# Optimization experiments

Hardware: AMD Instinct MI355X
Metric: run time of the kernel (lower is better)

The kernel has to match this reference:

```python
import jax, jax.numpy as jnp
import numpy as np

NEG_SLOPE = 0.2
EPS = 1e-5

N_NODES = 50000
N_GRAPHS = 500
NODES_PER_GRAPH = 100
N_EDGES = 500000
F_IN = 16
F_GRAPH = 4
HID = 64
N_CLASSES = 2


def setup_inputs() -> dict:
    key = jax.random.key(0)
    ks = jax.random.split(key, 32)
    x = jax.random.normal(ks[0], (N_NODES, F_IN), dtype=jnp.float32)
    # intra-graph random edges: dst lives in the same 100-node block as src
    src = jax.random.randint(ks[1], (N_EDGES,), 0, N_NODES)
    dst = (src // NODES_PER_GRAPH) * NODES_PER_GRAPH + jax.random.randint(ks[2], (N_EDGES,), 0, NODES_PER_GRAPH)
    edge_index = jnp.stack([src, dst]).astype(jnp.int64)
    graph_input = jax.random.normal(ks[3], (N_GRAPHS, F_GRAPH), dtype=jnp.float32)
    batch = (jnp.arange(N_NODES) // NODES_PER_GRAPH).astype(jnp.int64)

    def w(k, shape, scale=0.1):
        return (jax.random.normal(k, shape, dtype=jnp.float32) * scale)

    inp = dict(x=x, edge_index=edge_index, graph_input=graph_input, batch=batch)
    # GraphNorm params
    inp['gn_w'] = jnp.ones((F_IN,), jnp.float32)
    inp['gn_b'] = w(ks[4], (F_IN,))
    inp['gn_ms'] = jnp.ones((F_IN,), jnp.float32)
    inp['W1'] = w(ks[5], (F_IN, 4 * HID))
    inp['as1'] = w(ks[6], (4, HID)); inp['ad1'] = w(ks[7], (4, HID))
    inp['b1'] = w(ks[8], (4 * HID,))
    inp['W2'] = w(ks[9], (4 * HID, 4 * HID))
    inp['as2'] = w(ks[10], (4, HID)); inp['ad2'] = w(ks[11], (4, HID))
    inp['b2'] = w(ks[12], (4 * HID,))
    inp['W3'] = w(ks[13], (4 * HID, HID))
    inp['as3'] = w(ks[14], (1, HID)); inp['ad3'] = w(ks[15], (1, HID))
    inp['b3'] = w(ks[16], (HID,))
    # BatchNorm1d (eval mode) over [HID + F_GRAPH]
    D = HID + F_GRAPH
    inp['bn_g'] = 1.0 + w(ks[17], (D,))
    inp['bn_b'] = w(ks[18], (D,))
    inp['bn_m'] = jnp.zeros((D,), jnp.float32)
    inp['bn_v'] = jnp.ones((D,), jnp.float32)
    # Dense head
    inp['Wd1'] = w(ks[19], (D, HID)); inp['bd1'] = w(ks[20], (HID,))
    inp['Wd2'] = w(ks[21], (HID, HID)); inp['bd2'] = w(ks[22], (HID,))
    inp['Wo'] = w(ks[23], (HID, N_CLASSES)); inp['bo'] = w(ks[24], (N_CLASSES,))
    return inp


def _segment_softmax(e, seg, n):
    m = jax.ops.segment_max(e, seg, num_segments=n)
    ex = jnp.exp(e - m[seg])
    s = jax.ops.segment_sum(ex, seg, num_segments=n)
    return ex / s[seg]


def _gat_conv(x, src, dst, W, att_src, att_dst, b):
    N = x.shape[0]
    H, C = att_src.shape
    loop = jnp.arange(N)
    src = jnp.concatenate([src, loop])  # PyG GATConv adds self-loops
    dst = jnp.concatenate([dst, loop])
    h = (x @ W).reshape(N, H, C)
    a_src = (h * att_src).sum(-1)  # [N,H]
    a_dst = (h * att_dst).sum(-1)
    e = jax.nn.leaky_relu(a_src[src] + a_dst[dst], NEG_SLOPE)  # [E,H]
    alpha = _segment_softmax(e, dst, N)
    out = jax.ops.segment_sum(h[src] * alpha[:, :, None], dst, num_segments=N)
    return out.reshape(N, H * C) + b


def _graph_norm(x, batch, n_graphs, w, b, ms):
    cnt = jax.ops.segment_sum(jnp.ones((x.shape[0],), x.dtype), batch, num_segments=n_graphs)[:, None]
    mean = jax.ops.segment_sum(x, batch, num_segments=n_graphs) / cnt
    out = x - mean[batch] * ms
    var = jax.ops.segment_sum(out * out, batch, num_segments=n_graphs) / cnt
    return w * out / jnp.sqrt(var[batch] + EPS) + b


def _global_mean_pool(x, batch, n_graphs):
    cnt = jax.ops.segment_sum(jnp.ones((x.shape[0],), x.dtype), batch, num_segments=n_graphs)[:, None]
    return jax.ops.segment_sum(x, batch, num_segments=n_graphs) / cnt


def reference(x, edge_index, graph_input, batch,
              gn_w, gn_b, gn_ms,
              W1, as1, ad1, b1,
              W2, as2, ad2, b2,
              W3, as3, ad3, b3,
              bn_g, bn_b, bn_m, bn_v,
              Wd1, bd1, Wd2, bd2, Wo, bo):
    src, dst = edge_index[0], edge_index[1]
    G = graph_input.shape[0]
    h = _graph_norm(x, batch, G, gn_w, gn_b, gn_ms)
    # dropout is a no-op in eval
    h = jax.nn.elu(_gat_conv(h, src, dst, W1, as1, ad1, b1))
    h = jax.nn.elu(_gat_conv(h, src, dst, W2, as2, ad2, b2))
    h = _gat_conv(h, src, dst, W3, as3, ad3, b3)
    g = _global_mean_pool(h, batch, G)
    g = jnp.concatenate([g, graph_input], axis=1)
    g = (g - bn_m) / jnp.sqrt(bn_v + EPS) * bn_g + bn_b  # BatchNorm1d eval
    g = jax.nn.selu(g @ Wd1 + bd1)
    g = jax.nn.selu(g @ Wd2 + bd2)
    g = g @ Wo + bo
    return jax.nn.softmax(g, axis=1)
```

## Files before the change

kernel.cpp:

```cpp
#include <hip/hip_runtime.h>
#include <math.h>

#define N_NODES 50000
#define N_ROWS_PAD 50048
#define N_GRAPHS 500
#define NPG 100
#define N_EDGES 500000
#define F_IN 16
#define HID 64
#define EW_CAP 1408

#define SELU_SCALE 1.0507009873554804934193349852946f
#define SELU_ALPHA 1.6732632423543772848170429916717f

typedef __attribute__((ext_vector_type(8))) short short8;
typedef __attribute__((ext_vector_type(8))) unsigned short ushort8;
typedef __attribute__((ext_vector_type(4))) float floatx4;

__device__ __forceinline__ float lrelu(float x){ return x > 0.f ? x : 0.2f * x; }
__device__ __forceinline__ float eluf(float x){ return x > 0.f ? x : expf(x) - 1.f; }
__device__ __forceinline__ float seluf(float x){
    return x > 0.f ? SELU_SCALE * x : SELU_SCALE * (SELU_ALPHA * (expf(x) - 1.f));
}
__device__ __forceinline__ unsigned short f2bf(float x){
    unsigned u = __float_as_uint(x);
    return (unsigned short)((u + 0x7FFFu + ((u >> 16) & 1u)) >> 16);
}
__device__ __forceinline__ float bf2f(unsigned short u){
    return __uint_as_float((unsigned)u << 16);
}
__device__ __forceinline__ float bf2f_lo(unsigned u){
    return __uint_as_float(u << 16);
}
__device__ __forceinline__ float bf2f_hi(unsigned u){
    return __uint_as_float(u & 0xFFFF0000u);
}

__global__ void k_count(const int* __restrict__ dst, int* __restrict__ counts){
    int e = blockIdx.x * 256 + threadIdx.x;
    if (e < N_EDGES) atomicAdd(&counts[dst[e]], 1);
}

__global__ void __launch_bounds__(128)
k_local_scan(const int* __restrict__ counts, int* __restrict__ noff,
             int* __restrict__ cnt, int* __restrict__ write_ptr){
    __shared__ int s[128];
    int g = blockIdx.x, t = threadIdx.x;
    int v = (t < NPG) ? counts[g * NPG + t] : 0;
    s[t] = v; __syncthreads();
    for (int o = 1; o < 128; o <<= 1){
        int x = (t >= o) ? s[t - o] : 0;
        __syncthreads();
        s[t] += x;
        __syncthreads();
    }
    if (t < NPG){
        int excl = s[t] - v;
        noff[g * NPG + t] = excl;
        cnt[g * NPG + t] = v;
        write_ptr[g * NPG + t] = excl;
    }
}

__global__ void k_scatter(const int* __restrict__ src, const int* __restrict__ dst,
                          int* __restrict__ write_ptr, unsigned* __restrict__ csr){
    int e = blockIdx.x * 256 + threadIdx.x;
    if (e < N_EDGES){
        int d = dst[e];
        int g = d / NPG;
        int b = g * NPG;
        int pos = atomicAdd(&write_ptr[d], 1);
        csr[(size_t)g * EW_CAP + pos] = (unsigned)((src[e] - b) | ((d - b) << 8));
    }
}

__global__ void k_prep(const float* __restrict__ W1, const float* __restrict__ as1,
                       const float* __restrict__ ad1,
                       const float* __restrict__ W2, const float* __restrict__ as2,
                       const float* __restrict__ ad2,
                       const float* __restrict__ W3, const float* __restrict__ as3,
                       const float* __restrict__ ad3,
                       unsigned short* __restrict__ Wp2, unsigned short* __restrict__ Wp3,
                       float* __restrict__ M1f,
                       unsigned short* __restrict__ Mp2, unsigned short* __restrict__ Mp3){
    int id = blockIdx.x * 256 + threadIdx.x;
    if (id < 65536){
        int k = id >> 8, o = id & 255;
        int srccol = (o & 3) * 64 + (o >> 2);
        Wp2[(((k >> 3) * 256) + o) * 8 + (k & 7)] = f2bf(W2[k * 256 + srccol]);
    } else if (id < 81920){
        int i = id - 65536;
        int k = i >> 6, n = i & 63;
        Wp3[(((k >> 3) * 64) + n) * 8 + (k & 7)] = f2bf(W3[i]);
    } else if (id < 82048){
        int i = id - 81920;
        int k = i >> 3, j = i & 7;
        int h = j & 3;
        const float* a = (j < 4) ? as1 : ad1;
        float s = 0.f;
        for (int c = 0; c < 64; c++) s += W1[k * 256 + h * 64 + c] * a[h * 64 + c];
        M1f[k * 8 + j] = s;
    } else if (id < 86144){
        int i = id - 82048;
        int k = i >> 4, col = i & 15;
        float s = 0.f;
        if (col < 8){
            int h = col & 3;
            const float* a = (col < 4) ? as2 : ad2;
            for (int c = 0; c < 64; c++) s += W2[k * 256 + h * 64 + c] * a[h * 64 + c];
        }
        Mp2[((k >> 3) * 16 + col) * 8 + (k & 7)] = f2bf(s);
    } else if (id < 90240){
        int i = id - 86144;
        int k = i >> 4, col = i & 15;
        float s = 0.f;
        if (col < 2){
            const float* a = (col == 0) ? as3 : ad3;
            for (int c = 0; c < 64; c++) s += W3[k * 64 + c] * a[c];
        }
        Mp3[((k >> 3) * 16 + col) * 8 + (k & 7)] = f2bf(s);
    }
}

__global__ void __launch_bounds__(256)
k_gnorm_conv1(const float* __restrict__ x, const float* __restrict__ w,
              const float* __restrict__ b, const float* __restrict__ ms,
              const float* __restrict__ W1, const float* __restrict__ M1f,
              unsigned short* __restrict__ Ybf, float* __restrict__ lg1){
    __shared__ float sx[NPG * F_IN];
    __shared__ float Ws[16][256];
    __shared__ float red[16][16];
    __shared__ float meanS[16], varS[16];
    int g = blockIdx.x, t = threadIdx.x;
    int base = g * NPG;
    for (int idx = t; idx < NPG * F_IN; idx += 256) sx[idx] = x[base * F_IN + idx];
    for (int i = t; i < 1024; i += 256)
        *(float4*)&Ws[0][i * 4] = *(const float4*)&W1[i * 4];
    __syncthreads();
    int f = t & 15, grp = t >> 4;
    float p = 0.f;
    for (int i = grp; i < NPG; i += 16) p += sx[i * 16 + f];
    red[grp][f] = p; __syncthreads();
    if (t < 16){
        float s = 0.f;
        for (int i = 0; i < 16; i++) s += red[i][t];
        meanS[t] = s * (1.f / 100.f);
    }
    __syncthreads();
    float mm = meanS[f] * ms[f];
    p = 0.f;
    for (int i = grp; i < NPG; i += 16){ float v = sx[i * 16 + f] - mm; p += v * v; }
    red[grp][f] = p; __syncthreads();
    if (t < 16){
        float s = 0.f;
        for (int i = 0; i < 16; i++) s += red[i][t];
        varS[t] = s * (1.f / 100.f);
    }
    __syncthreads();
    for (int idx = t; idx < NPG * F_IN; idx += 256){
        int ff = idx & 15;
        sx[idx] = w[ff] * (sx[idx] - meanS[ff] * ms[ff]) * rsqrtf(varS[ff] + 1e-5f) + b[ff];
    }
    __syncthreads();
    int c4 = t & 15, rsub = t >> 4;
    for (int n = rsub; n < NPG; n += 16){
        float acc[16];
        #pragma unroll
        for (int j = 0; j < 16; j++) acc[j] = 0.f;
        #pragma unroll
        for (int k = 0; k < 16; k++){
            float a_ = sx[n * 16 + k];
            float4 b0 = *(const float4*)&Ws[k][c4 * 4];
            float4 b1 = *(const float4*)&Ws[k][64 + c4 * 4];
            float4 b2 = *(const float4*)&Ws[k][128 + c4 * 4];
            float4 b3 = *(const float4*)&Ws[k][192 + c4 * 4];
            float bv[16] = {b0.x, b0.y, b0.z, b0.w, b1.x, b1.y, b1.z, b1.w,
                            b2.x, b2.y, b2.z, b2.w, b3.x, b3.y, b3.z, b3.w};
            #pragma unroll
            for (int j = 0; j < 16; j++) acc[j] = fmaf(a_, bv[j], acc[j]);
        }
        ushort8 ua, ub;
        #pragma unroll
        for (int m = 0; m < 8; m++){
            ua[m] = f2bf(acc[(m & 3) * 4 + (m >> 2)]);
            ub[m] = f2bf(acc[(m & 3) * 4 + 2 + (m >> 2)]);
        }
        size_t ob = (size_t)(base + n) * 256 + c4 * 16;
        *(ushort8*)&Ybf[ob]     = ua;
        *(ushort8*)&Ybf[ob + 8] = ub;
    }
    for (int i = t; i < NPG * 8; i += 256){
        int n = i >> 3, j = i & 7;
        float s = 0.f;
        #pragma unroll
        for (int ff = 0; ff < 16; ff++) s += sx[n * 16 + ff] * M1f[ff * 8 + j];
        lg1[(size_t)(base + n) * 8 + j] = s;
    }
}

template<int COLB, int LG>
__global__ void __launch_bounds__(256)
k_gemm_mfma(const unsigned short* __restrict__ Xb,
            const unsigned short* __restrict__ Wp,
            const unsigned short* __restrict__ Mp,
            unsigned short* __restrict__ Ybf, float* __restrict__ lg,
            int N, int K, int OUT){
    int b = blockIdx.x;
    if (COLB == 4){
        int xcd = b & 7, idx = b >> 3;
        b = xcd * (int)(gridDim.x >> 3) + idx;
    }
    int cb = b & (COLB - 1);
    int rb = b / COLB;

    int t = threadIdx.x;
    int wave = t >> 6, lane = t & 63;
    int quad = lane >> 4, ln = lane & 15;
    int r0 = rb * 64 + wave * 16;
    int c0 = cb * 64;

    floatx4 acc[4];
    #pragma unroll
    for (int f = 0; f < 4; f++) acc[f] = (floatx4){0.f, 0.f, 0.f, 0.f};
    floatx4 accL = (floatx4){0.f, 0.f, 0.f, 0.f};

    const unsigned short* aptr = Xb + (size_t)(r0 + ln) * K + quad * 8;
    for (int kt = 0; kt < K; kt += 32){
        short8 a = *(const short8*)(aptr + kt);
        int kc = (kt >> 3) + quad;
        #pragma unroll
        for (int f = 0; f < 4; f++){
            short8 bfr = *(const short8*)(Wp + ((size_t)kc * OUT + c0 + f * 16 + ln) * 8);
            acc[f] = __builtin_amdgcn_mfma_f32_16x16x32_bf16(a, bfr, acc[f], 0, 0, 0);
        }
        if (LG > 0){
            if (cb == 0){
                short8 m = *(const short8*)(Mp + ((size_t)kc * 16 + ln) * 8);
                accL = __builtin_amdgcn_mfma_f32_16x16x32_bf16(a, m, accL, 0, 0, 0);
            }
        }
    }
    int rowb = r0 + quad * 4;
    #pragma unroll
    for (int f = 0; f < 4; f++){
        int col = c0 + f * 16 + ln;
        #pragma unroll
        for (int rg = 0; rg < 4; rg++){
            int row = rowb + rg;
            if (row < N) Ybf[(size_t)row * OUT + col] = f2bf(acc[f][rg]);
        }
    }
    if (LG > 0){
        if (cb == 0 && ln < LG){
            #pragma unroll
            for (int rg = 0; rg < 4; rg++){
                int row = rowb + rg;
                if (row < N) lg[(size_t)row * LG + ln] = accL[rg];
            }
        }
    }
}

__global__ void __launch_bounds__(512)
k_fused4(const unsigned short* __restrict__ hbf, const float* __restrict__ lg,
         const float* __restrict__ bias,
         const unsigned* __restrict__ csr, const int* __restrict__ noff,
         const int* __restrict__ cnt, unsigned short* __restrict__ out_bf){
    __shared__ __align__(16) unsigned int edl[EW_CAP][4];
    __shared__ __align__(16) float asrcl[NPG * 4], adstl[NPG * 4];
    __shared__ __align__(16) float wselfl[NPG * 4], rsuml[NPG * 4];
    __shared__ int offl[NPG], cntl[NPG];

    int g = blockIdx.x, t = threadIdx.x;
    int wave = t >> 6, lane = t & 63;
    int base = g * NPG;
    size_t ebeg = (size_t)g * EW_CAP;

    if (t < NPG){
        offl[t] = noff[base + t];
        cntl[t] = cnt[base + t];
        const float* lp = lg + (size_t)(base + t) * 8;
        *(float4*)&asrcl[t * 4] = *(const float4*)lp;
        *(float4*)&adstl[t * 4] = *(const float4*)(lp + 4);
    }
    __syncthreads();
    int eln = offl[NPG - 1] + cntl[NPG - 1];
    for (int i = t; i < eln; i += 512) edl[i][2] = csr[ebeg + i];
    __syncthreads();

    for (int i = t; i < eln; i += 512){
        unsigned sd = edl[i][2];
        int s = sd & 0xFF, d = sd >> 8;
        float4 av = *(const float4*)&asrcl[s * 4];
        float4 dv = *(const float4*)&adstl[d * 4];
        unsigned w0 = f2bf(expf(lrelu(av.x + dv.x)));
        unsigned w1 = f2bf(expf(lrelu(av.y + dv.y)));
        unsigned w2 = f2bf(expf(lrelu(av.z + dv.z)));
        unsigned w3 = f2bf(expf(lrelu(av.w + dv.w)));
        edl[i][0] = w0 | (w1 << 16);
        edl[i][1] = w2 | (w3 << 16);
    }
    __syncthreads();

    if (t < NPG){
        int d = t;
        float4 av = *(const float4*)&asrcl[d * 4];
        float4 dv = *(const float4*)&adstl[d * 4];
        float ws0 = expf(lrelu(av.x + dv.x));
        float ws1 = expf(lrelu(av.y + dv.y));
        float ws2 = expf(lrelu(av.z + dv.z));
        float ws3 = expf(lrelu(av.w + dv.w));
        float s0 = ws0, s1 = ws1, s2 = ws2, s3 = ws3;
        int ebg = offl[d], n = cntl[d];
        for (int j = 0; j < n; j++){
            uint2 v = *(const uint2*)&edl[ebg + j][0];
            s0 += bf2f_lo(v.x); s1 += bf2f_hi(v.x);
            s2 += bf2f_lo(v.y); s3 += bf2f_hi(v.y);
        }
        *(float4*)&wselfl[d * 4] = make_float4(ws0, ws1, ws2, ws3);
        *(float4*)&rsuml[d * 4]  = make_float4(1.f / s0, 1.f / s1, 1.f / s2, 1.f / s3);
    }
    __syncthreads();

    float b0 = bias[lane], b1 = bias[64 + lane], b2 = bias[128 + lane], b3 = bias[192 + lane];
    for (int d = wave; d < NPG; d += 8){
        float4 ws = *(const float4*)&wselfl[d * 4];
        float4 rs = *(const float4*)&rsuml[d * 4];
        ushort4 hv = *(const ushort4*)&hbf[(size_t)(base + d) * 256 + lane * 4];
        float a0 = ws.x * bf2f(hv.x);
        float a1 = ws.y * bf2f(hv.y);
        float a2 = ws.z * bf2f(hv.z);
        float a3 = ws.w * bf2f(hv.w);
        int ebg = offl[d], n = cntl[d];
        int j = 0;
        #pragma unroll 1
        for (; j + 4 <= n; j += 4){
            #pragma unroll
            for (int k = 0; k < 4; k++){
                uint4 v = *(const uint4*)&edl[ebg + j + k][0];
                int s = (int)(v.z & 0xFFu);
                ushort4 x = *(const ushort4*)&hbf[(size_t)(base + s) * 256 + lane * 4];
                a0 = fmaf(bf2f_lo(v.x), bf2f(x.x), a0);
                a1 = fmaf(bf2f_hi(v.x), bf2f(x.y), a1);
                a2 = fmaf(bf2f_lo(v.y), bf2f(x.z), a2);
                a3 = fmaf(bf2f_hi(v.y), bf2f(x.w), a3);
            }
        }
        for (; j < n; j++){
            uint4 v = *(const uint4*)&edl[ebg + j][0];
            int s = (int)(v.z & 0xFFu);
            ushort4 x = *(const ushort4*)&hbf[(size_t)(base + s) * 256 + lane * 4];
            a0 = fmaf(bf2f_lo(v.x), bf2f(x.x), a0);
            a1 = fmaf(bf2f_hi(v.x), bf2f(x.y), a1);
            a2 = fmaf(bf2f_lo(v.y), bf2f(x.z), a2);
            a3 = fmaf(bf2f_hi(v.y), bf2f(x.w), a3);
        }
        size_t ob = (size_t)(base + d) * 256 + lane;
        out_bf[ob]       = f2bf(eluf(a0 * rs.x + b0));
        out_bf[ob + 64]  = f2bf(eluf(a1 * rs.y + b1));
        out_bf[ob + 128] = f2bf(eluf(a2 * rs.z + b2));
        out_bf[ob + 192] = f2bf(eluf(a3 * rs.w + b3));
    }
}

__global__ void __launch_bounds__(512)
k_tail(const unsigned short* __restrict__ xb, const unsigned short* __restrict__ Wp3,
       const unsigned short* __restrict__ Mp3, const float* __restrict__ bias,
       const unsigned* __restrict__ csr, const int* __restrict__ noff,
       const int* __restrict__ cnt, const float* __restrict__ gin,
       const float* __restrict__ bn_g, const float* __restrict__ bn_b,
       const float* __restrict__ bn_m, const float* __restrict__ bn_v,
       const float* __restrict__ Wd1, const float* __restrict__ bd1,
       const float* __restrict__ Wd2, const float* __restrict__ bd2,
       const float* __restrict__ Wo, const float* __restrict__ bo,
       float* __restrict__ out){
    __shared__ __align__(16) unsigned short h3[NPG * 64];
    __shared__ __align__(16) unsigned int edl[EW_CAP][2];
    __shared__ float asrcl[NPG], adstl[NPG];
    __shared__ float wselfl[NPG], rsuml[NPG];
    __shared__ int offl[NPG], cntl[NPG];
    __shared__ float red[8][64];
    __shared__ float gv[68], g2[64], g3[64];

    int g = blockIdx.x, t = threadIdx.x;
    int wave = t >> 6, lane = t & 63;
    int base = g * NPG;
    size_t ebeg = (size_t)g * EW_CAP;

    if (wave < 7){
        int quad = lane >> 4, ln = lane & 15;
        floatx4 acc[4];
        #pragma unroll
        for (int f = 0; f < 4; f++) acc[f] = (floatx4){0.f, 0.f, 0.f, 0.f};
        floatx4 accL = (floatx4){0.f, 0.f, 0.f, 0.f};
        const unsigned short* aptr = xb + (size_t)(base + wave * 16 + ln) * 256 + quad * 8;
        for (int kt = 0; kt < 256; kt += 32){
            short8 a = *(const short8*)(aptr + kt);
            int kc = (kt >> 3) + quad;
            #pragma unroll
            for (int f = 0; f < 4; f++){
                short8 bfr = *(const short8*)(Wp3 + ((size_t)kc * 64 + f * 16 + ln) * 8);
                acc[f] = __builtin_amdgcn_mfma_f32_16x16x32_bf16(a, bfr, acc[f], 0, 0, 0);
            }
            short8 m = *(const short8*)(Mp3 + ((size_t)kc * 16 + ln) * 8);
            accL = __builtin_amdgcn_mfma_f32_16x16x32_bf16(a, m, accL, 0, 0, 0);
        }
        int rowb = wave * 16 + quad * 4;
        #pragma unroll
        for (int f = 0; f < 4; f++){
            int col = f * 16 + ln;
            #pragma unroll
            for (int rg = 0; rg < 4; rg++){
                int row = rowb + rg;
                if (row < NPG) h3[row * 64 + col] = f2bf(acc[f][rg]);
            }
        }
        if (ln < 2){
            #pragma unroll
            for (int rg = 0; rg < 4; rg++){
                int row = rowb + rg;
                if (row < NPG){
                    if (ln == 0) asrcl[row] = accL[rg];
                    else         adstl[row] = accL[rg];
                }
            }
        }
    } else {
        for (int i = lane; i < NPG; i += 64){
            offl[i] = noff[base + i];
            cntl[i] = cnt[base + i];
        }
        int el = noff[base + NPG - 1] + cnt[base + NPG - 1];
        for (int i = lane; i < el; i += 64) edl[i][1] = csr[ebeg + i];
    }
    __syncthreads();
    int eln = offl[NPG - 1] + cntl[NPG - 1];

    for (int i = t; i < eln; i += 512){
        unsigned sd = edl[i][1];
        int s = sd & 0xFF, d = sd >> 8;
        edl[i][0] = (unsigned)f2bf(expf(lrelu(asrcl[s] + adstl[d])));
    }
    __syncthreads();

    if (t < NPG){
        float wsf = expf(lrelu(asrcl[t] + adstl[t]));
        float sum = wsf;
        int ebg = offl[t], n = cntl[t];
        for (int j = 0; j < n; j++) sum += bf2f((unsigned short)edl[ebg + j][0]);
        wselfl[t] = wsf;
        rsuml[t] = 1.f / sum;
    }
    __syncthreads();

    float bl = bias[lane];
    float pool = 0.f;
    for (int d = wave; d < NPG; d += 8){
        float acc = wselfl[d] * bf2f(h3[d * 64 + lane]);
        int ebg = offl[d], n = cntl[d];
        for (int j = 0; j < n; j++){
            uint2 v = *(const uint2*)&edl[ebg + j][0];
            acc = fmaf(bf2f_lo(v.x), bf2f(h3[(int)(v.y & 0xFFu) * 64 + lane]), acc);
        }
        pool += acc * rsuml[d] + bl;
    }
    red[wave][lane] = pool;
    __syncthreads();

    if (t < 64){
        float s = 0.f;
        #pragma unroll
        for (int i = 0; i < 8; i++) s += red[i][t];
        float mean = s * (1.f / 100.f);
        gv[t] = (mean - bn_m[t]) * rsqrtf(bn_v[t] + 1e-5f) * bn_g[t] + bn_b[t];
    } else if (t < 68){
        int j = t - 64;
        float v = gin[g * 4 + j];
        gv[t] = (v - bn_m[t]) * rsqrtf(bn_v[t] + 1e-5f) * bn_g[t] + bn_b[t];
    }
    __syncthreads();
    if (t < 64){
        float s = bd1[t];
        for (int i = 0; i < 68; i++) s += gv[i] * Wd1[i * 64 + t];
        g2[t] = seluf(s);
    }
    __syncthreads();
    if (t < 64){
        float s = bd2[t];
        for (int i = 0; i < 64; i++) s += g2[i] * Wd2[i * 64 + t];
        g3[t] = seluf(s);
    }
    __syncthreads();
    if (t == 0){
        float l0 = bo[0], l1 = bo[1];
        for (int i = 0; i < 64; i++){ l0 += g3[i] * Wo[i * 2]; l1 += g3[i] * Wo[i * 2 + 1]; }
        float mx = fmaxf(l0, l1);
        float e0 = expf(l0 - mx), e1 = expf(l1 - mx);
        float inv = 1.f / (e0 + e1);
        out[g * 2] = e0 * inv;
        out[g * 2 + 1] = e1 * inv;
    }
}

extern "C" void kernel_launch(void* const* d_in, const int* in_sizes, int n_in,
                              void* d_out, int out_size, void* d_ws, size_t ws_size,
                              hipStream_t stream){
    const float* x   = (const float*)d_in[0];
    const int*   ei  = (const int*)d_in[1];
    const float* gin = (const float*)d_in[2];
    const float* gn_w = (const float*)d_in[4];
    const float* gn_b = (const float*)d_in[5];
    const float* gn_ms = (const float*)d_in[6];
    const float* W1 = (const float*)d_in[7];
    const float* as1 = (const float*)d_in[8];
    const float* ad1 = (const float*)d_in[9];
    const float* b1 = (const float*)d_in[10];
    const float* W2 = (const float*)d_in[11];
    const float* as2 = (const float*)d_in[12];
    const float* ad2 = (const float*)d_in[13];
    const float* b2 = (const float*)d_in[14];
    const float* W3 = (const float*)d_in[15];
    const float* as3 = (const float*)d_in[16];
    const float* ad3 = (const float*)d_in[17];
    const float* b3 = (const float*)d_in[18];
    const float* bn_g = (const float*)d_in[19];
    const float* bn_b = (const float*)d_in[20];
    const float* bn_m = (const float*)d_in[21];
    const float* bn_v = (const float*)d_in[22];
    const float* Wd1 = (const float*)d_in[23];
    const float* bd1 = (const float*)d_in[24];
    const float* Wd2 = (const float*)d_in[25];
    const float* bd2 = (const float*)d_in[26];
    const float* Wo = (const float*)d_in[27];
    const float* bo = (const float*)d_in[28];
    float* out = (float*)d_out;

    const int* src = ei;
    const int* dst = ei + N_EDGES;

    char* ws = (char*)d_ws;
    size_t off = 0;
    auto alloc = [&](size_t bytes) -> void* {
        void* p = ws + off;
        off = (off + bytes + 255) & ~(size_t)255;
        return p;
    };
    int* counts     = (int*)alloc((size_t)N_NODES * 4);
    int* write_ptr  = (int*)alloc((size_t)N_NODES * 4);
    unsigned* csr   = (unsigned*)alloc((size_t)N_GRAPHS * EW_CAP * 4);
    int* noff       = (int*)alloc((size_t)N_NODES * 4);
    int* cnt        = (int*)alloc((size_t)N_NODES * 4);
    unsigned short* wp2 = (unsigned short*)alloc((size_t)256 * 256 * 2);
    unsigned short* wp3 = (unsigned short*)alloc((size_t)256 * 64 * 2);
    float* M1f      = (float*)alloc((size_t)16 * 8 * 4);
    unsigned short* Mp2 = (unsigned short*)alloc((size_t)32 * 16 * 8 * 2);
    unsigned short* Mp3 = (unsigned short*)alloc((size_t)32 * 16 * 8 * 2);
    float* lg1      = (float*)alloc((size_t)N_NODES * 8 * 4);
    float* lg2      = (float*)alloc((size_t)N_ROWS_PAD * 8 * 4);
    unsigned short* xbh = (unsigned short*)alloc((size_t)N_NODES * 256 * 2);
    unsigned short* xb  = (unsigned short*)alloc((size_t)N_ROWS_PAD * 256 * 2);

    hipMemsetAsync(counts, 0, (size_t)N_NODES * 4, stream);
    k_count<<<(N_EDGES + 255) / 256, 256, 0, stream>>>(dst, counts);
    k_prep<<<(90240 + 255) / 256, 256, 0, stream>>>(W1, as1, ad1, W2, as2, ad2,
                                                    W3, as3, ad3, wp2, wp3, M1f, Mp2, Mp3);
    k_local_scan<<<N_GRAPHS, 128, 0, stream>>>(counts, noff, cnt, write_ptr);
    k_scatter<<<(N_EDGES + 255) / 256, 256, 0, stream>>>(src, dst, write_ptr, csr);

    k_gnorm_conv1<<<N_GRAPHS, 256, 0, stream>>>(x, gn_w, gn_b, gn_ms, W1, M1f, xbh, lg1);
    k_fused4<<<N_GRAPHS, 512, 0, stream>>>(xbh, lg1, b1, csr, noff, cnt, xb);

    k_gemm_mfma<4, 8><<<(N_ROWS_PAD / 64) * 4, 256, 0, stream>>>(xb, wp2, Mp2, xbh, lg2,
                                                                 N_NODES, 256, 256);
    k_fused4<<<N_GRAPHS, 512, 0, stream>>>(xbh, lg2, b2, csr, noff, cnt, xb);

    k_tail<<<N_GRAPHS, 512, 0, stream>>>(xb, wp3, Mp3, b3, csr, noff, cnt, gin,
                                         bn_g, bn_b, bn_m, bn_v,
                                         Wd1, bd1, Wd2, bd2, Wo, bo, out);
}
```

Measured before the change: 315.8 us.

## Fuse layer-2 GEMM with GAT aggregation into per-graph kernel using LDS

Replaces the separate MFMA GEMM kernel and the second k_fused4 aggregation with one per-graph kernel, k_mid. Seven waves compute the 100x256 projection and attention logits straight into shared memory while the eighth wave loads the edge list. The block then computes edge weights, softmax sums and the neighbour gather from LDS. This removes the global round trip of the projected features and logits plus one launch. In exchange each block needs a large LDS footprint (about 51KB for features) and 16 accumulators per wave, which lowers occupancy, and every block reloads the whole weight matrix.

```diff
diff --git a/kernel.cpp b/kernel.cpp
--- a/kernel.cpp
+++ b/kernel.cpp
@@ -198,69 +198,6 @@
     }
 }
 
-template<int COLB, int LG>
-__global__ void __launch_bounds__(256)
-k_gemm_mfma(const unsigned short* __restrict__ Xb,
-            const unsigned short* __restrict__ Wp,
-            const unsigned short* __restrict__ Mp,
-            unsigned short* __restrict__ Ybf, float* __restrict__ lg,
-            int N, int K, int OUT){
-    int b = blockIdx.x;
-    if (COLB == 4){
-        int xcd = b & 7, idx = b >> 3;
-        b = xcd * (int)(gridDim.x >> 3) + idx;
-    }
-    int cb = b & (COLB - 1);
-    int rb = b / COLB;
-
-    int t = threadIdx.x;
-    int wave = t >> 6, lane = t & 63;
-    int quad = lane >> 4, ln = lane & 15;
-    int r0 = rb * 64 + wave * 16;
-    int c0 = cb * 64;
-
-    floatx4 acc[4];
-    #pragma unroll
-    for (int f = 0; f < 4; f++) acc[f] = (floatx4){0.f, 0.f, 0.f, 0.f};
-    floatx4 accL = (floatx4){0.f, 0.f, 0.f, 0.f};
-
-    const unsigned short* aptr = Xb + (size_t)(r0 + ln) * K + quad * 8;
-    for (int kt = 0; kt < K; kt += 32){
-        short8 a = *(const short8*)(aptr + kt);
-        int kc = (kt >> 3) + quad;
-        #pragma unroll
-        for (int f = 0; f < 4; f++){
-            short8 bfr = *(const short8*)(Wp + ((size_t)kc * OUT + c0 + f * 16 + ln) * 8);
-            acc[f] = __builtin_amdgcn_mfma_f32_16x16x32_bf16(a, bfr, acc[f], 0, 0, 0);
-        }
-        if (LG > 0){
-            if (cb == 0){
-                short8 m = *(const short8*)(Mp + ((size_t)kc * 16 + ln) * 8);
-                accL = __builtin_amdgcn_mfma_f32_16x16x32_bf16(a, m, accL, 0, 0, 0);
-            }
-        }
-    }
-    int rowb = r0 + quad * 4;
-    #pragma unroll
-    for (int f = 0; f < 4; f++){
-        int col = c0 + f * 16 + ln;
-        #pragma unroll
-        for (int rg = 0; rg < 4; rg++){
-            int row = rowb + rg;
-            if (row < N) Ybf[(size_t)row * OUT + col] = f2bf(acc[f][rg]);
-        }
-    }
-    if (LG > 0){
-        if (cb == 0 && ln < LG){
-            #pragma unroll
-            for (int rg = 0; rg < 4; rg++){
-                int row = rowb + rg;
-                if (row < N) lg[(size_t)row * LG + ln] = accL[rg];
-            }
-        }
-    }
-}
-
 __global__ void __launch_bounds__(512)
 k_fused4(const unsigned short* __restrict__ hbf, const float* __restrict__ lg,
          const float* __restrict__ bias,
@@ -350,6 +287,147 @@
             uint4 v = *(const uint4*)&edl[ebg + j][0];
             int s = (int)(v.z & 0xFFu);
             ushort4 x = *(const ushort4*)&hbf[(size_t)(base + s) * 256 + lane * 4];
+            a0 = fmaf(bf2f_lo(v.x), bf2f(x.x), a0);
+            a1 = fmaf(bf2f_hi(v.x), bf2f(x.y), a1);
+            a2 = fmaf(bf2f_lo(v.y), bf2f(x.z), a2);
+            a3 = fmaf(bf2f_hi(v.y), bf2f(x.w), a3);
+        }
+        size_t ob = (size_t)(base + d) * 256 + lane;
+        out_bf[ob]       = f2bf(eluf(a0 * rs.x + b0));
+        out_bf[ob + 64]  = f2bf(eluf(a1 * rs.y + b1));
+        out_bf[ob + 128] = f2bf(eluf(a2 * rs.z + b2));
+        out_bf[ob + 192] = f2bf(eluf(a3 * rs.w + b3));
+    }
+}
+
+__global__ void __launch_bounds__(512)
+k_mid(const unsigned short* __restrict__ xbin, const unsigned short* __restrict__ Wp2,
+      const unsigned short* __restrict__ Mp2, const float* __restrict__ bias,
+      const unsigned* __restrict__ csr, const int* __restrict__ noff,
+      const int* __restrict__ cnt, unsigned short* __restrict__ out_bf){
+    __shared__ __align__(16) unsigned short hl[NPG * 256];
+    __shared__ __align__(16) unsigned int edw[EW_CAP][2];
+    __shared__ unsigned short eds[EW_CAP];
+    __shared__ __align__(16) float asrcl[NPG * 4], adstl[NPG * 4];
+    __shared__ __align__(16) float wselfl[NPG * 4], rsuml[NPG * 4];
+    __shared__ int offl[NPG], cntl[NPG];
+
+    int g = blockIdx.x, t = threadIdx.x;
+    int wave = t >> 6, lane = t & 63;
+    int base = g * NPG;
+    size_t ebeg = (size_t)g * EW_CAP;
+
+    if (wave < 7){
+        int quad = lane >> 4, ln = lane & 15;
+        floatx4 acc[16];
+        #pragma unroll
+        for (int f = 0; f < 16; f++) acc[f] = (floatx4){0.f, 0.f, 0.f, 0.f};
+        floatx4 accL = (floatx4){0.f, 0.f, 0.f, 0.f};
+        const unsigned short* aptr = xbin + (size_t)(base + wave * 16 + ln) * 256 + quad * 8;
+        for (int kt = 0; kt < 256; kt += 32){
+            short8 a = *(const short8*)(aptr + kt);
+            int kc = (kt >> 3) + quad;
+            #pragma unroll
+            for (int f = 0; f < 16; f++){
+                short8 bfr = *(const short8*)(Wp2 + ((size_t)kc * 256 + f * 16 + ln) * 8);
+                acc[f] = __builtin_amdgcn_mfma_f32_16x16x32_bf16(a, bfr, acc[f], 0, 0, 0);
+            }
+            short8 m = *(const short8*)(Mp2 + ((size_t)kc * 16 + ln) * 8);
+            accL = __builtin_amdgcn_mfma_f32_16x16x32_bf16(a, m, accL, 0, 0, 0);
+        }
+        int rowb = wave * 16 + quad * 4;
+        #pragma unroll
+        for (int f = 0; f < 16; f++){
+            int col = f * 16 + ln;
+            #pragma unroll
+            for (int rg = 0; rg < 4; rg++){
+                int row = rowb + rg;
+                if (row < NPG) hl[row * 256 + col] = f2bf(acc[f][rg]);
+            }
+        }
+        if (ln < 8){
+            #pragma unroll
+            for (int rg = 0; rg < 4; rg++){
+                int row = rowb + rg;
+                if (row < NPG){
+                    if (ln < 4) asrcl[row * 4 + ln] = accL[rg];
+                    else        adstl[row * 4 + (ln - 4)] = accL[rg];
+                }
+            }
+        }
+    } else {
+        for (int i = lane; i < NPG; i += 64){
+            offl[i] = noff[base + i];
+            cntl[i] = cnt[base + i];
+        }
+        int el = noff[base + NPG - 1] + cnt[base + NPG - 1];
+        for (int i = lane; i < el; i += 64) eds[i] = (unsigned short)csr[ebeg + i];
+    }
+    __syncthreads();
+    int eln = offl[NPG - 1] + cntl[NPG - 1];
+
+    for (int i = t; i < eln; i += 512){
+        unsigned sd = eds[i];
+        int s = sd & 0xFF, d = sd >> 8;
+        float4 av = *(const float4*)&asrcl[s * 4];
+        float4 dv = *(const float4*)&adstl[d * 4];
+        unsigned w0 = f2bf(expf(lrelu(av.x + dv.x)));
+        unsigned w1 = f2bf(expf(lrelu(av.y + dv.y)));
+        unsigned w2 = f2bf(expf(lrelu(av.z + dv.z)));
+        unsigned w3 = f2bf(expf(lrelu(av.w + dv.w)));
+        edw[i][0] = w0 | (w1 << 16);
+        edw[i][1] = w2 | (w3 << 16);
+    }
+    __syncthreads();
+
+    if (t < NPG){
+        int d = t;
+        float4 av = *(const float4*)&asrcl[d * 4];
+        float4 dv = *(const float4*)&adstl[d * 4];
+        float ws0 = expf(lrelu(av.x + dv.x));
+        float ws1 = expf(lrelu(av.y + dv.y));
+        float ws2 = expf(lrelu(av.z + dv.z));
+        float ws3 = expf(lrelu(av.w + dv.w));
+        float s0 = ws0, s1 = ws1, s2 = ws2, s3 = ws3;
+        int ebg = offl[d], n = cntl[d];
+        for (int j = 0; j < n; j++){
+            uint2 v = *(const uint2*)&edw[ebg + j][0];
+            s0 += bf2f_lo(v.x); s1 += bf2f_hi(v.x);
+            s2 += bf2f_lo(v.y); s3 += bf2f_hi(v.y);
+        }
+        *(float4*)&wselfl[d * 4] = make_float4(ws0, ws1, ws2, ws3);
+        *(float4*)&rsuml[d * 4]  = make_float4(1.f / s0, 1.f / s1, 1.f / s2, 1.f / s3);
+    }
+    __syncthreads();
+
+    float b0 = bias[lane], b1 = bias[64 + lane], b2 = bias[128 + lane], b3 = bias[192 + lane];
+    for (int d = wave; d < NPG; d += 8){
+        float4 ws = *(const float4*)&wselfl[d * 4];
+        float4 rs = *(const float4*)&rsuml[d * 4];
+        ushort4 hv = *(const ushort4*)&hl[d * 256 + lane * 4];
+        float a0 = ws.x * bf2f(hv.x);
+        float a1 = ws.y * bf2f(hv.y);
+        float a2 = ws.z * bf2f(hv.z);
+        float a3 = ws.w * bf2f(hv.w);
+        int ebg = offl[d], n = cntl[d];
+        int j = 0;
+        #pragma unroll 1
+        for (; j + 4 <= n; j += 4){
+            #pragma unroll
+            for (int k = 0; k < 4; k++){
+                int s = (int)(eds[ebg + j + k] & 0xFFu);
+                uint2 v = *(const uint2*)&edw[ebg + j + k][0];
+                ushort4 x = *(const ushort4*)&hl[s * 256 + lane * 4];
+                a0 = fmaf(bf2f_lo(v.x), bf2f(x.x), a0);
+                a1 = fmaf(bf2f_hi(v.x), bf2f(x.y), a1);
+                a2 = fmaf(bf2f_lo(v.y), bf2f(x.z), a2);
+                a3 = fmaf(bf2f_hi(v.y), bf2f(x.w), a3);
+            }
+        }
+        for (; j < n; j++){
+            int s = (int)(eds[ebg + j] & 0xFFu);
+            uint2 v = *(const uint2*)&edw[ebg + j][0];
+            ushort4 x = *(const ushort4*)&hl[s * 256 + lane * 4];
             a0 = fmaf(bf2f_lo(v.x), bf2f(x.x), a0);
             a1 = fmaf(bf2f_hi(v.x), bf2f(x.y), a1);
             a2 = fmaf(bf2f_lo(v.y), bf2f(x.z), a2);
@@ -556,8 +634,7 @@
     unsigned short* Mp2 = (unsigned short*)alloc((size_t)32 * 16 * 8 * 2);
     unsigned short* Mp3 = (unsigned short*)alloc((size_t)32 * 16 * 8 * 2);
     float* lg1      = (float*)alloc((size_t)N_NODES * 8 * 4);
-    float* lg2      = (float*)alloc((size_t)N_ROWS_PAD * 8 * 4);
-    unsigned short* xbh = (unsigned short*)alloc((size_t)N_NODES * 256 * 2);
+    unsigned short* xbh = (unsigned short*)alloc((size_t)N_ROWS_PAD * 256 * 2);
     unsigned short* xb  = (unsigned short*)alloc((size_t)N_ROWS_PAD * 256 * 2);
 
     hipMemsetAsync(counts, 0, (size_t)N_NODES * 4, stream);
@@ -570,11 +647,9 @@
     k_gnorm_conv1<<<N_GRAPHS, 256, 0, stream>>>(x, gn_w, gn_b, gn_ms, W1, M1f, xbh, lg1);
     k_fused4<<<N_GRAPHS, 512, 0, stream>>>(xbh, lg1, b1, csr, noff, cnt, xb);
 
-    k_gemm_mfma<4, 8><<<(N_ROWS_PAD / 64) * 4, 256, 0, stream>>>(xb, wp2, Mp2, xbh, lg2,
-                                                                 N_NODES, 256, 256);
-    k_fused4<<<N_GRAPHS, 512, 0, stream>>>(xbh, lg2, b2, csr, noff, cnt, xb);
-
-    k_tail<<<N_GRAPHS, 512, 0, stream>>>(xb, wp3, Mp3, b3, csr, noff, cnt, gin,
+    k_mid<<<N_GRAPHS, 512, 0, stream>>>(xb, wp2, Mp2, b2, csr, noff, cnt, xbh);
+
+    k_tail<<<N_GRAPHS, 512, 0, stream>>>(xbh, wp3, Mp3, b3, csr, noff, cnt, gin,
                                          bn_g, bn_b, bn_m, bn_v,
                                          Wd1, bd1, Wd2, bd2, Wo, bo, out);
 }
```

Result: faster. 307.7 us (median of 2 runs) (-2.6%).
